# Performance work log

Hardware: AMD Instinct MI355X
Metric: run time of the kernel (lower is better)

The kernel has to match this reference:

```python
import jax, jax.numpy as jnp
import numpy as np

B_, S_, E_ = 1, 2048, 2048
NH, P_, N_, G_, K_, CS = 64, 64, 128, 1, 4, 256
INTER = NH * P_            # 4096
CONV_DIM = INTER + 2 * G_ * N_  # 4352
PROJ = INTER + CONV_DIM + NH
EPS = 1e-5


def setup_inputs() -> dict:
    key = jax.random.key(0)
    ks = jax.random.split(key, 6)
    return {
        "input_states": jax.random.normal(ks[0], (B_, S_, E_), dtype=jnp.float32),
        "mask": jnp.ones((B_, 1, S_), dtype=jnp.int32),
        "W_in": jax.random.normal(ks[1], (PROJ, E_), dtype=jnp.float32) * 0.02,
        "conv_w": jax.random.normal(ks[2], (CONV_DIM, K_), dtype=jnp.float32) * 0.2,
        "conv_b": jnp.zeros((CONV_DIM,), dtype=jnp.float32),
        "dt_bias": jnp.ones((NH,), dtype=jnp.float32),
        "A_log": jnp.log(jnp.arange(1, NH + 1, dtype=jnp.float32)),
        "D": jnp.ones((NH,), dtype=jnp.float32),
        "norm_w": jnp.ones((INTER,), dtype=jnp.float32),
        "W_out": jax.random.normal(ks[3], (E_, INTER), dtype=jnp.float32) * 0.02,
    }


def segsum(x):
    # x: [..., L]; out[..., i, j] = sum_{j < k <= i} x[..., k], -inf above diagonal
    L = x.shape[-1]
    i = jnp.arange(L)
    strict = i[:, None] > i[None, :]
    X = jnp.where(strict, x[..., :, None], 0.0)   # [..., L(i), L(j)]
    S = jnp.cumsum(X, axis=-2)
    return jnp.where(i[:, None] >= i[None, :], S, -jnp.inf)


def reference(input_states, mask, W_in, conv_w, conv_b, dt_bias, A_log, D, norm_w, W_out):
    B, S, E = input_states.shape
    # mask has shape[1]==1 -> apply_mask_to_padding_states is a no-op
    proj = input_states @ W_in.T                      # [B,S,PROJ]
    gate = proj[..., :INTER]
    h_BC = proj[..., INTER:INTER + CONV_DIM]
    dt = proj[..., INTER + CONV_DIM:]                 # [B,S,NH]

    # causal depthwise conv1d (padding=K-1, truncated to seq_len)
    xpad = jnp.pad(h_BC, ((0, 0), (K_ - 1, 0), (0, 0)))
    conv = conv_b
    for i in range(K_):
        conv = conv + xpad[:, i:i + S, :] * conv_w[:, i]
    h_BC = jax.nn.silu(conv)

    hidden = h_BC[..., :INTER]
    Bm = h_BC[..., INTER:INTER + G_ * N_]
    Cm = h_BC[..., INTER + G_ * N_:]

    A = -jnp.exp(A_log)                               # [NH]
    dt = jnp.clip(jax.nn.softplus(dt + dt_bias), 0.0) # [B,S,NH]

    Hs = hidden.reshape(B, S, NH, P_).astype(jnp.float32)
    Bm = jnp.tile(Bm.reshape(B, S, G_, N_).astype(jnp.float32), (1, 1, NH // G_, 1))
    Cm = jnp.tile(Cm.reshape(B, S, G_, N_).astype(jnp.float32), (1, 1, NH // G_, 1))

    D_resid = D[None, None, :, None] * Hs             # pad=0 since S % CS == 0
    Hdt = Hs * dt[..., None]
    At = A * dt                                       # [B,S,NH]

    C_ = S // CS
    Hc = Hdt.reshape(B, C_, CS, NH, P_)
    Ac = At.reshape(B, C_, CS, NH)
    Bc = Bm.reshape(B, C_, CS, NH, N_)
    Cc = Cm.reshape(B, C_, CS, NH, N_)

    Ap = jnp.transpose(Ac, (0, 3, 1, 2))              # [B,H,C,L]
    A_cum = jnp.cumsum(Ap, axis=-1)                   # [B,H,C,L]
    L_tri = jnp.exp(segsum(Ap))                       # [B,H,C,L,L]

    # diagonal (intra-chunk) output
    Gm = jnp.einsum('bclhn,bcshn->bclsh', Cc, Bc)
    M = Gm * jnp.transpose(L_tri, (0, 2, 3, 4, 1))    # [B,C,L,S,H]
    Yd = jnp.einsum('bclsh,bcshp->bclhp', M, Hc)

    # per-chunk states (note: source uses same-chunk states, no inter-chunk scan)
    decay = jnp.exp(A_cum[..., -1:] - A_cum)          # [B,H,C,L]
    Bd = Bc * jnp.transpose(decay, (0, 2, 3, 1))[..., None]
    states = jnp.einsum('bclhn,bclhp->bchpn', Bd, Hc) # [B,C,H,P,N]

    Sd = jnp.transpose(jnp.exp(A_cum), (0, 2, 3, 1))  # [B,C,L,H]
    Yoff = jnp.einsum('bclhn,bchpn->bclhp', Cc, states) * Sd[..., None]

    y = (Yd + Yoff).reshape(B, S, NH, P_) + D_resid
    y = y.reshape(B, S, INTER)

    # gated RMSNorm (fp32)
    yf = y.astype(jnp.float32) * jax.nn.silu(gate.astype(jnp.float32))
    var = jnp.mean(yf * yf, axis=-1, keepdims=True)
    yn = norm_w * (yf * jax.lax.rsqrt(var + EPS))

    return yn @ W_out.T
```

## Files before the change

### kernel.cpp

```cpp
#include <hip/hip_runtime.h>
#include <math.h>

#define S_LEN   2048
#define E_DIM   2048
#define NH      64
#define P_DIM   64
#define N_DIM   128
#define CS      256
#define NCHUNK  8
#define INTER   4096
#define CONVD   4352
#define PROJ    8512
#define GEMM1N  8448
#define EPS     1e-5f

#define OFF_PROJBF 0ull
#define OFF_HBC    8650752ull
#define OFF_DTG    13107200ull
#define OFF_DTPART 13238272ull
#define OFF_GM     17432576ull
#define OFF_YV     17956864ull
#define OFF_R      26345472ull
#define OFF_WOUT   37093376ull

typedef __bf16 bf16x8 __attribute__((ext_vector_type(8)));
typedef float  f32x4  __attribute__((ext_vector_type(4)));
typedef float  f32x16 __attribute__((ext_vector_type(16)));

__device__ __forceinline__ float bf2f(unsigned short u) {
    union { unsigned int i; float f; } v; v.i = ((unsigned int)u) << 16; return v.f;
}
__device__ __forceinline__ unsigned short f2bf(float f) {
    union { float f; unsigned int i; } v; v.f = f;
    unsigned int r = v.i + 0x7FFFu + ((v.i >> 16) & 1u);
    return (unsigned short)(r >> 16);
}
__device__ __forceinline__ void gl_lds16(const void* g, void* l) {
    __builtin_amdgcn_global_load_lds(
        (const __attribute__((address_space(1))) void*)g,
        (__attribute__((address_space(3))) void*)l, 16, 0, 0);
}

__global__ __launch_bounds__(256) void cast3_kernel(
    const float* __restrict__ X, const float* __restrict__ Win,
    const float* __restrict__ Wout, unsigned short* __restrict__ Xbf,
    unsigned short* __restrict__ Winbf, unsigned short* __restrict__ Woutbf)
{
    const int blk = blockIdx.x;
    const float* src; unsigned short* dst; size_t off;
    if (blk < 2048)       { src = X;    dst = Xbf;    off = (size_t)blk * 2048; }
    else if (blk < 10496) { src = Win;  dst = Winbf;  off = (size_t)(blk - 2048) * 2048; }
    else                  { src = Wout; dst = Woutbf; off = (size_t)(blk - 10496) * 2048; }
    size_t i = off + (size_t)threadIdx.x * 8;
    float4 a = *(const float4*)(src + i);
    float4 b = *(const float4*)(src + i + 4);
    uint4 o;
    o.x = (unsigned int)f2bf(a.x) | ((unsigned int)f2bf(a.y) << 16);
    o.y = (unsigned int)f2bf(a.z) | ((unsigned int)f2bf(a.w) << 16);
    o.z = (unsigned int)f2bf(b.x) | ((unsigned int)f2bf(b.y) << 16);
    o.w = (unsigned int)f2bf(b.z) | ((unsigned int)f2bf(b.w) << 16);
    *(uint4*)(dst + i) = o;
}

__global__ __launch_bounds__(256) void gemm_bt_mfma(
    const unsigned short* __restrict__ A, int lda, long long sA,
    const unsigned short* __restrict__ B, int ldb, long long sB,
    float* __restrict__ Cf, unsigned short* __restrict__ Cb, int ldc,
    long long sC, int K, int mswap)
{
    __shared__ unsigned short As[128 * 64];
    __shared__ unsigned short Bs[128 * 64];
    A += (long long)blockIdx.z * sA;
    B += (long long)blockIdx.z * sB;
    const int t     = threadIdx.x;
    const int m0    = (mswap ? blockIdx.x : blockIdx.y) * 128;
    const int n0    = (mswap ? blockIdx.y : blockIdx.x) * 128;
    const int w     = t >> 6;
    const int lane  = t & 63;
    const int col   = lane & 31;
    const int khalf = lane >> 5;
    const int wm    = (w & 1) * 64;
    const int wn    = (w >> 1) * 64;

    const int srow  = t >> 3;
    const int sslot = t & 7;
    const unsigned short* Agp[4];
    const unsigned short* Bgp[4];
#pragma unroll
    for (int i = 0; i < 4; i++) {
        const int r   = srow + 32 * i;
        const int gch = sslot ^ ((r ^ (r >> 3)) & 7);
        Agp[i] = A + (size_t)(m0 + r) * lda + gch * 8;
        Bgp[i] = B + (size_t)(n0 + r) * ldb + gch * 8;
    }
    unsigned short* Asl = &As[t * 8];
    unsigned short* Bsl = &Bs[t * 8];

    int aOff[2], aXor[2], bOff[2], bXor[2];
#pragma unroll
    for (int i = 0; i < 2; i++) {
        const int ra = wm + i * 32 + col;
        aOff[i] = ra * 64; aXor[i] = (ra ^ (ra >> 3)) & 7;
        const int rb = wn + i * 32 + col;
        bOff[i] = rb * 64; bXor[i] = (rb ^ (rb >> 3)) & 7;
    }

    f32x16 acc[2][2];
#pragma unroll
    for (int mi = 0; mi < 2; mi++)
#pragma unroll
        for (int ni = 0; ni < 2; ni++)
#pragma unroll
            for (int e = 0; e < 16; e++) acc[mi][ni][e] = 0.f;

    for (int k0 = 0; k0 < K; k0 += 64) {
        __syncthreads();
#pragma unroll
        for (int i = 0; i < 4; i++) {
            gl_lds16(Agp[i] + k0, Asl + i * 2048);
            gl_lds16(Bgp[i] + k0, Bsl + i * 2048);
        }
        __syncthreads();
#pragma unroll
        for (int ks = 0; ks < 4; ks++) {
            const int ch = ks * 2 + khalf;
            bf16x8 af[2], bfr[2];
#pragma unroll
            for (int i = 0; i < 2; i++) {
                af[i]  = *(const bf16x8*)&As[aOff[i] + ((ch ^ aXor[i]) * 8)];
                bfr[i] = *(const bf16x8*)&Bs[bOff[i] + ((ch ^ bXor[i]) * 8)];
            }
#pragma unroll
            for (int mi = 0; mi < 2; mi++)
#pragma unroll
                for (int ni = 0; ni < 2; ni++)
                    acc[mi][ni] = __builtin_amdgcn_mfma_f32_32x32x16_bf16(
                        af[mi], bfr[ni], acc[mi][ni], 0, 0, 0);
        }
    }

    if (Cb) {
#pragma unroll
        for (int mi = 0; mi < 2; mi++)
#pragma unroll
            for (int ni = 0; ni < 2; ni++) {
                const int rbase = m0 + wm + mi * 32 + 4 * khalf;
                const int cc    = n0 + wn + ni * 32 + col;
#pragma unroll
                for (int g = 0; g < 4; g++)
#pragma unroll
                    for (int rr = 0; rr < 4; rr++)
                        Cb[(size_t)(rbase + 8 * g + rr) * ldc + cc] =
                            f2bf(acc[mi][ni][4 * g + rr]);
            }
    } else {
        float* Cz = Cf + (long long)blockIdx.z * sC;
#pragma unroll
        for (int mi = 0; mi < 2; mi++)
#pragma unroll
            for (int ni = 0; ni < 2; ni++) {
                const int rbase = m0 + wm + mi * 32 + 4 * khalf;
                const int cc    = n0 + wn + ni * 32 + col;
#pragma unroll
                for (int g = 0; g < 4; g++)
#pragma unroll
                    for (int rr = 0; rr < 4; rr++)
                        Cz[(size_t)(rbase + 8 * g + rr) * ldc + cc] =
                            acc[mi][ni][4 * g + rr];
            }
    }
}

__global__ __launch_bounds__(256) void addf4_kernel(
    const float* __restrict__ p, float* __restrict__ o)
{
    size_t i = ((size_t)blockIdx.x * 256 + threadIdx.x) * 4;
    float4 a = *(const float4*)(p + i);
    float4 b = *(const float4*)(p + i + 4194304);
    float4 c = *(const float4*)(p + i + 8388608);
    float4 d = *(const float4*)(p + i + 12582912);
    float4 r = make_float4(a.x + b.x + c.x + d.x, a.y + b.y + c.y + d.y,
                           a.z + b.z + c.z + d.z, a.w + b.w + c.w + d.w);
    *(float4*)(o + i) = r;
}

__global__ __launch_bounds__(256) void gemm_nt(
    const float* __restrict__ A, int lda, long long sA,
    const float* __restrict__ B, int ldb, long long sB,
    float* __restrict__ C, int ldc, long long sC, int K)
{
    A += (long long)blockIdx.z * sA;
    B += (long long)blockIdx.z * sB;
    C += (long long)blockIdx.z * sC;
    const int t  = threadIdx.x;
    const int m0 = blockIdx.y * 128;
    const int n0 = blockIdx.x * 64;
    __shared__ float As[16][132];
    __shared__ float Bs[16][68];
    const int tx = t & 15;
    const int ty = t >> 4;

    const int arow = t & 127;
    const int akh  = (t >> 7) * 8;
    const float* Aload = A + (size_t)(m0 + arow) * (size_t)lda + akh;
    const int brow = t & 63;
    const int bk4  = (t >> 6) * 4;
    const float* Bload = B + (size_t)(n0 + brow) * (size_t)ldb + bk4;

    float acc[8][4];
#pragma unroll
    for (int i = 0; i < 8; i++)
#pragma unroll
        for (int j = 0; j < 4; j++) acc[i][j] = 0.f;

    for (int k0 = 0; k0 < K; k0 += 16) {
        __syncthreads();
        float4 a0 = *(const float4*)(Aload + k0);
        float4 a1 = *(const float4*)(Aload + k0 + 4);
        float4 b0 = *(const float4*)(Bload + k0);
        As[akh + 0][arow] = a0.x; As[akh + 1][arow] = a0.y;
        As[akh + 2][arow] = a0.z; As[akh + 3][arow] = a0.w;
        As[akh + 4][arow] = a1.x; As[akh + 5][arow] = a1.y;
        As[akh + 6][arow] = a1.z; As[akh + 7][arow] = a1.w;
        Bs[bk4 + 0][brow] = b0.x; Bs[bk4 + 1][brow] = b0.y;
        Bs[bk4 + 2][brow] = b0.z; Bs[bk4 + 3][brow] = b0.w;
        __syncthreads();
#pragma unroll
        for (int k = 0; k < 16; k++) {
            float4 a4 = *(const float4*)(&As[k][ty * 8]);
            float4 a5 = *(const float4*)(&As[k][ty * 8 + 4]);
            float4 b4 = *(const float4*)(&Bs[k][tx * 4]);
            float am[8] = {a4.x, a4.y, a4.z, a4.w, a5.x, a5.y, a5.z, a5.w};
            float bn[4] = {b4.x, b4.y, b4.z, b4.w};
#pragma unroll
            for (int i = 0; i < 8; i++)
#pragma unroll
                for (int j = 0; j < 4; j++) acc[i][j] += am[i] * bn[j];
        }
    }
#pragma unroll
    for (int i = 0; i < 8; i++) {
        float4 o = make_float4(acc[i][0], acc[i][1], acc[i][2], acc[i][3]);
        *(float4*)(C + (size_t)(m0 + ty * 8 + i) * (size_t)ldc + n0 + tx * 4) = o;
    }
}

__global__ __launch_bounds__(256) void dt_reduce_kernel(
    const float* __restrict__ part, const float* __restrict__ dt_bias,
    float* __restrict__ dtg)
{
    const int i = blockIdx.x * 256 + threadIdx.x;
    float x = dt_bias[i & 63];
#pragma unroll
    for (int z = 0; z < 32; z++) x += part[(size_t)z * 131072 + i];
    dtg[i] = (x > 20.f) ? x : log1pf(__expf(x));
}

__global__ __launch_bounds__(256) void conv_silu8_kernel(
    const unsigned short* __restrict__ projbf, const float* __restrict__ conv_w,
    const float* __restrict__ conv_b, unsigned short* __restrict__ out)
{
    const int c  = blockIdx.x * 256 + threadIdx.x;
    const int s0 = blockIdx.y * 8;
    const float4 w = *(const float4*)(conv_w + (size_t)c * 4);
    const float b = conv_b[c];
    const size_t base = 4096 + (size_t)c;
    float v[11];
#pragma unroll
    for (int m = 0; m < 11; m++) {
        int s = s0 - 3 + m;
        v[m] = (s >= 0) ? bf2f(projbf[(size_t)s * GEMM1N + base]) : 0.f;
    }
#pragma unroll
    for (int j = 0; j < 8; j++) {
        float acc = b + v[j] * w.x + v[j + 1] * w.y + v[j + 2] * w.z + v[j + 3] * w.w;
        float sig = 1.f / (1.f + __expf(-acc));
        out[(size_t)(s0 + j) * CONVD + c] = f2bf(acc * sig);
    }
}

__global__ __launch_bounds__(256, 2) void ssm_mfma_kernel(
    const unsigned short* __restrict__ hBC, const float* __restrict__ dtg,
    const float* __restrict__ Gm, const float* __restrict__ A_log,
    const float* __restrict__ Dp, float* __restrict__ y)
{
    const int h    = blockIdx.x;
    const int c    = blockIdx.y;
    const int t    = threadIdx.x;
    const int wid  = t >> 6;
    const int lane = t & 63;
    const int lo   = lane & 15;
    const int q    = lane >> 4;

    __shared__ float sAcum[CS], sdt[CS], sD[CS], sEs[CS], sDecay[CS], sScl[CS];
    __shared__ float sWaveSum[4];
    __shared__ unsigned short sHdtT[64 * 264];
    __shared__ unsigned short sStT[64 * 136];
    __shared__ unsigned short sBufB[128 * 72];

    const float A = -__expf(A_log[h]);
    const int row0 = c * CS;
    const unsigned short* hid = hBC + (size_t)row0 * CONVD + h * P_DIM;
    const unsigned short* Bp  = hBC + (size_t)row0 * CONVD + INTER;
    const unsigned short* Cp  = hBC + (size_t)row0 * CONVD + INTER + N_DIM;
    const float* gm = Gm + (size_t)c * CS * CS;

    float dtv = dtg[(size_t)(row0 + t) * NH + h];
    float v = A * dtv;
    for (int off = 1; off < 64; off <<= 1) {
        float u = __shfl_up(v, off, 64);
        if (lane >= off) v += u;
    }
    if (lane == 63) sWaveSum[wid] = v;
    __syncthreads();
    float pre = 0.f;
    for (int i = 0; i < 4; i++) if (i < wid) pre += sWaveSum[i];
    v += pre;
    sAcum[t] = v;
    sdt[t] = dtv;
    __syncthreads();
    const float AcumEnd = sAcum[CS - 1];
    {
        float ac   = sAcum[t];
        float apre = (t < 64) ? 0.f : sAcum[(t & ~63) - 1];
        sD[t]     = __expf(ac - apre);
        sEs[t]    = __expf(sAcum[t | 63] - ac);
        sDecay[t] = __expf(AcumEnd - ac);
        sScl[t]   = __expf(ac);
    }

    unsigned short* stgu = sStT;
    for (int lt = 0; lt < 4; lt++) {
        __syncthreads();
        {
            const int c8 = (t & 7) * 8;
#pragma unroll
            for (int j = 0; j < 2; j++) {
                int l = (t >> 3) + 32 * j;
                *(uint4*)&stgu[l * 64 + c8] =
                    *(const uint4*)(hid + (size_t)(lt * 64 + l) * CONVD + c8);
            }
        }
        __syncthreads();
        {
            const int p = t & 63, lq = (t >> 6) * 16;
#pragma unroll
            for (int j = 0; j < 4; j++) {
                ushort4 pk;
                int l0 = lq + j * 4;
                pk.x = f2bf(bf2f(stgu[(l0 + 0) * 64 + p]) * sdt[lt * 64 + l0 + 0]);
                pk.y = f2bf(bf2f(stgu[(l0 + 1) * 64 + p]) * sdt[lt * 64 + l0 + 1]);
                pk.z = f2bf(bf2f(stgu[(l0 + 2) * 64 + p]) * sdt[lt * 64 + l0 + 2]);
                pk.w = f2bf(bf2f(stgu[(l0 + 3) * 64 + p]) * sdt[lt * 64 + l0 + 3]);
                *(uint2*)&sHdtT[p * 264 + lt * 64 + l0] = *(uint2*)&pk;
            }
        }
    }

    f32x4 acc2[2][4];
#pragma unroll
    for (int mi = 0; mi < 2; mi++)
#pragma unroll
        for (int ni = 0; ni < 4; ni++) acc2[mi][ni] = (f32x4){0.f, 0.f, 0.f, 0.f};
    const int psub = (wid & 1) * 32;
    const int nsub = (wid >> 1) * 64;

    for (int qt = 0; qt < 4; qt++) {
        for (int hf = 0; hf < 2; hf++) {
            __syncthreads();
            {
                const int n8 = (t & 15) * 8;
#pragma unroll
                for (int j = 0; j < 2; j++) {
                    int r = (t >> 4) + 16 * j;
                    *(uint4*)&stgu[r * 128 + n8] =
                        *(const uint4*)(Bp + (size_t)(qt * 64 + hf * 32 + r) * CONVD + n8);
                }
            }
            __syncthreads();
            {
                const int n = t & 127, lc = (t >> 7) * 16;
#pragma unroll
                for (int j = 0; j < 4; j++) {
                    int l0 = lc + j * 4;
                    ushort4 pk;
                    pk.x = f2bf(bf2f(stgu[(l0 + 0) * 128 + n]) * sDecay[qt * 64 + hf * 32 + l0 + 0]);
                    pk.y = f2bf(bf2f(stgu[(l0 + 1) * 128 + n]) * sDecay[qt * 64 + hf * 32 + l0 + 1]);
                    pk.z = f2bf(bf2f(stgu[(l0 + 2) * 128 + n]) * sDecay[qt * 64 + hf * 32 + l0 + 2]);
                    pk.w = f2bf(bf2f(stgu[(l0 + 3) * 128 + n]) * sDecay[qt * 64 + hf * 32 + l0 + 3]);
                    *(uint2*)&sBufB[n * 72 + hf * 32 + l0] = *(uint2*)&pk;
                }
            }
        }
        __syncthreads();
#pragma unroll
        for (int ks = 0; ks < 2; ks++) {
            const int k0 = qt * 64 + ks * 32;
            const int kq = ks * 32;
            bf16x8 a2[2], b2[4];
#pragma unroll
            for (int mi = 0; mi < 2; mi++)
                a2[mi] = *(const bf16x8*)&sHdtT[(psub + mi * 16 + lo) * 264 + k0 + q * 8];
#pragma unroll
            for (int ni = 0; ni < 4; ni++)
                b2[ni] = *(const bf16x8*)&sBufB[(nsub + ni * 16 + lo) * 72 + kq + q * 8];
#pragma unroll
            for (int mi = 0; mi < 2; mi++)
#pragma unroll
                for (int ni = 0; ni < 4; ni++)
                    acc2[mi][ni] = __builtin_amdgcn_mfma_f32_16x16x32_bf16(
                        a2[mi], b2[ni], acc2[mi][ni], 0, 0, 0);
        }
    }
    __syncthreads();
#pragma unroll
    for (int mi = 0; mi < 2; mi++)
#pragma unroll
        for (int ni = 0; ni < 4; ni++)
#pragma unroll
            for (int rr = 0; rr < 4; rr++) {
                int p = psub + mi * 16 + q * 4 + rr;
                int n = nsub + ni * 16 + lo;
                sStT[p * 136 + n] = f2bf(acc2[mi][ni][rr]);
            }

    f32x4 accY[4][2][2];
#pragma unroll
    for (int i = 0; i < 4; i++)
#pragma unroll
        for (int mi = 0; mi < 2; mi++)
#pragma unroll
            for (int pi = 0; pi < 2; pi++) accY[i][mi][pi] = (f32x4){0.f, 0.f, 0.f, 0.f};
    const int pcol = (wid & 1) * 32;
    const int rsub = (wid >> 1) * 16;
    unsigned short* Cs = sBufB;

    for (int i = 0; i < 4; i++) {
        __syncthreads();
        {
            const int n8 = (t & 15) * 8;
#pragma unroll
            for (int j = 0; j < 4; j++) {
                int r = (t >> 4) + 16 * j;
                uint4 cv = *(const uint4*)(Cp + (size_t)(i * 64 + r) * CONVD + n8);
                float scl = sScl[i * 64 + r];
                const unsigned short* cu = (const unsigned short*)&cv;
                ushort4 p0, p1;
                p0.x = f2bf(bf2f(cu[0]) * scl); p0.y = f2bf(bf2f(cu[1]) * scl);
                p0.z = f2bf(bf2f(cu[2]) * scl); p0.w = f2bf(bf2f(cu[3]) * scl);
                p1.x = f2bf(bf2f(cu[4]) * scl); p1.y = f2bf(bf2f(cu[5]) * scl);
                p1.z = f2bf(bf2f(cu[6]) * scl); p1.w = f2bf(bf2f(cu[7]) * scl);
                *(uint2*)&Cs[r * 136 + n8]     = *(uint2*)&p0;
                *(uint2*)&Cs[r * 136 + n8 + 4] = *(uint2*)&p1;
            }
        }
        __syncthreads();
#pragma unroll
        for (int ks = 0; ks < 4; ks++) {
            const int k0 = ks * 32;
            bf16x8 a3[2], b3[2];
#pragma unroll
            for (int mi = 0; mi < 2; mi++)
                a3[mi] = *(const bf16x8*)&Cs[(mi * 32 + rsub + lo) * 136 + k0 + q * 8];
#pragma unroll
            for (int pi = 0; pi < 2; pi++)
                b3[pi] = *(const bf16x8*)&sStT[(pcol + pi * 16 + lo) * 136 + k0 + q * 8];
#pragma unroll
            for (int mi = 0; mi < 2; mi++)
#pragma unroll
                for (int pi = 0; pi < 2; pi++)
                    accY[i][mi][pi] = __builtin_amdgcn_mfma_f32_16x16x32_bf16(
                        a3[mi], b3[pi], accY[i][mi][pi], 0, 0, 0);
        }
    }

    unsigned short* Mt = sBufB;
    for (int i = 0; i < 4; i++) {
        const int nk = 2 * (i + 1);
        for (int mi = 0; mi < 2; mi++) {
            __syncthreads();
            if (wid <= i) {
                float P = 1.f;
                for (int m = wid + 1; m <= i - 1; m++) P *= sD[m * 64 + 63];
                const int s4 = wid * 64 + lo * 4;
                float4 es4 = *(const float4*)&sEs[s4];
#pragma unroll
                for (int j = 0; j < 8; j++) {
                    int lr = q + j * 4;
                    int l  = i * 64 + mi * 32 + lr;
                    float4 g4 = *(const float4*)&gm[(size_t)l * CS + s4];
                    float w0, w1, w2, w3;
                    if (wid == i) {
                        float al = sAcum[l];
                        w0 = (s4 + 0 <= l) ? __expf(al - sAcum[s4 + 0]) : 0.f;
                        w1 = (s4 + 1 <= l) ? __expf(al - sAcum[s4 + 1]) : 0.f;
                        w2 = (s4 + 2 <= l) ? __expf(al - sAcum[s4 + 2]) : 0.f;
                        w3 = (s4 + 3 <= l) ? __expf(al - sAcum[s4 + 3]) : 0.f;
                    } else {
                        float rs = sD[l] * P;
                        w0 = rs * es4.x; w1 = rs * es4.y;
                        w2 = rs * es4.z; w3 = rs * es4.w;
                    }
                    ushort4 pk;
                    pk.x = f2bf(g4.x * w0); pk.y = f2bf(g4.y * w1);
                    pk.z = f2bf(g4.z * w2); pk.w = f2bf(g4.w * w3);
                    *(uint2*)&Mt[lr * 264 + s4] = *(uint2*)&pk;
                }
            }
            __syncthreads();
            for (int ks = 0; ks < nk; ks++) {
                const int k0 = ks * 32;
                bf16x8 am = *(const bf16x8*)&Mt[(rsub + lo) * 264 + k0 + q * 8];
                bf16x8 b1[2];
#pragma unroll
                for (int pi = 0; pi < 2; pi++)
                    b1[pi] = *(const bf16x8*)&sHdtT[(pcol + pi * 16 + lo) * 264 + k0 + q * 8];
#pragma unroll
                for (int pi = 0; pi < 2; pi++)
                    accY[i][mi][pi] = __builtin_amdgcn_mfma_f32_16x16x32_bf16(
                        am, b1[pi], accY[i][mi][pi], 0, 0, 0);
            }
        }
    }

    const float Dh = Dp[h];
#pragma unroll
    for (int i = 0; i < 4; i++)
#pragma unroll
        for (int mi = 0; mi < 2; mi++)
#pragma unroll
            for (int pi = 0; pi < 2; pi++)
#pragma unroll
                for (int rr = 0; rr < 4; rr++) {
                    int l = i * 64 + mi * 32 + rsub + q * 4 + rr;
                    int p = pcol + pi * 16 + lo;
                    float hv = bf2f(hid[(size_t)l * CONVD + p]);
                    y[(size_t)(row0 + l) * INTER + h * P_DIM + p] =
                        accY[i][mi][pi][rr] + Dh * hv;
                }
}

__global__ __launch_bounds__(256) void norm_kernel(
    const float* __restrict__ y, const unsigned short* __restrict__ projbf,
    const float* __restrict__ norm_w, unsigned short* __restrict__ yn)
{
    const int s = blockIdx.x;
    const int t = threadIdx.x;
    __shared__ float sYf[INTER];
    __shared__ float sW[4];
    const float* yrow = y + (size_t)s * INTER;
    const unsigned short* grow = projbf + (size_t)s * GEMM1N;
    float sum = 0.f;
    for (int j0 = 0; j0 < INTER; j0 += 2048) {
        int j = j0 + t * 8;
        float4 y0 = *(const float4*)(yrow + j);
        float4 y1 = *(const float4*)(yrow + j + 4);
        uint4 gp = *(const uint4*)(grow + j);
        float gv[8] = {
            bf2f((unsigned short)(gp.x & 0xffff)), bf2f((unsigned short)(gp.x >> 16)),
            bf2f((unsigned short)(gp.y & 0xffff)), bf2f((unsigned short)(gp.y >> 16)),
            bf2f((unsigned short)(gp.z & 0xffff)), bf2f((unsigned short)(gp.z >> 16)),
            bf2f((unsigned short)(gp.w & 0xffff)), bf2f((unsigned short)(gp.w >> 16))};
        float yv8[8] = {y0.x, y0.y, y0.z, y0.w, y1.x, y1.y, y1.z, y1.w};
#pragma unroll
        for (int e = 0; e < 8; e++) {
            float f = yv8[e] * (gv[e] / (1.f + __expf(-gv[e])));
            sum += f * f;
            sYf[j + e] = f;
        }
    }
    for (int off = 32; off > 0; off >>= 1) sum += __shfl_down(sum, off, 64);
    if ((t & 63) == 0) sW[t >> 6] = sum;
    __syncthreads();
    const float var = (sW[0] + sW[1] + sW[2] + sW[3]) * (1.f / (float)INTER);
    const float rs = rsqrtf(var + EPS);
    for (int j0 = 0; j0 < INTER; j0 += 2048) {
        int j = j0 + t * 8;
        float4 w0 = *(const float4*)(norm_w + j);
        float4 w1 = *(const float4*)(norm_w + j + 4);
        float wv[8] = {w0.x, w0.y, w0.z, w0.w, w1.x, w1.y, w1.z, w1.w};
        unsigned short o[8];
#pragma unroll
        for (int e = 0; e < 8; e++) o[e] = f2bf(sYf[j + e] * wv[e] * rs);
        uint4 ov;
        ov.x = (unsigned int)o[0] | ((unsigned int)o[1] << 16);
        ov.y = (unsigned int)o[2] | ((unsigned int)o[3] << 16);
        ov.z = (unsigned int)o[4] | ((unsigned int)o[5] << 16);
        ov.w = (unsigned int)o[6] | ((unsigned int)o[7] << 16);
        *(uint4*)(yn + (size_t)s * INTER + j) = ov;
    }
}

extern "C" void kernel_launch(void* const* d_in, const int* in_sizes, int n_in,
                              void* d_out, int out_size, void* d_ws, size_t ws_size,
                              hipStream_t stream)
{
    const float* X       = (const float*)d_in[0];
    const float* W_in    = (const float*)d_in[2];
    const float* conv_w  = (const float*)d_in[3];
    const float* conv_b  = (const float*)d_in[4];
    const float* dt_bias = (const float*)d_in[5];
    const float* A_log   = (const float*)d_in[6];
    const float* Dp      = (const float*)d_in[7];
    const float* norm_w  = (const float*)d_in[8];
    const float* W_out   = (const float*)d_in[9];
    float* out = (float*)d_out;
    float* ws  = (float*)d_ws;

    unsigned short* projbf = (unsigned short*)(ws + OFF_PROJBF);
    unsigned short* hbc16  = (unsigned short*)(ws + OFF_HBC);
    float* dtg     = ws + OFF_DTG;
    float* dtpart  = ws + OFF_DTPART;
    float* gm      = ws + OFF_GM;
    float* yv      = ws + OFF_YV;
    unsigned short* Xbf    = (unsigned short*)(ws + OFF_R);
    unsigned short* Winbf  = (unsigned short*)(ws + OFF_R + 2097152);
    unsigned short* ynbf   = (unsigned short*)(ws + OFF_R);
    unsigned short* Woutbf = (unsigned short*)(ws + OFF_WOUT);
    float* part = ws;

    cast3_kernel<<<14592, 256, 0, stream>>>(X, W_in, W_out, Xbf, Winbf, Woutbf);

    gemm_bt_mfma<<<dim3(S_LEN / 128, GEMM1N / 128, 1), 256, 0, stream>>>(
        Xbf, E_DIM, 0LL, Winbf, E_DIM, 0LL, nullptr, projbf, GEMM1N, 0LL,
        E_DIM, 1);

    gemm_nt<<<dim3(1, 16, 32), 256, 0, stream>>>(
        X, E_DIM, 64LL, W_in + (size_t)GEMM1N * E_DIM, E_DIM, 64LL,
        dtpart, NH, 131072LL, 64);
    dt_reduce_kernel<<<512, 256, 0, stream>>>(dtpart, dt_bias, dtg);

    conv_silu8_kernel<<<dim3(CONVD / 256, S_LEN / 8), 256, 0, stream>>>(
        projbf, conv_w, conv_b, hbc16);

    gemm_bt_mfma<<<dim3(CS / 128, CS / 128, NCHUNK), 256, 0, stream>>>(
        hbc16 + INTER + N_DIM, CONVD, (long long)CS * CONVD,
        hbc16 + INTER,         CONVD, (long long)CS * CONVD,
        gm, nullptr, CS, (long long)CS * CS, N_DIM, 0);

    ssm_mfma_kernel<<<dim3(NH, NCHUNK), 256, 0, stream>>>(
        hbc16, dtg, gm, A_log, Dp, yv);

    norm_kernel<<<dim3(S_LEN), 256, 0, stream>>>(yv, projbf, norm_w, ynbf);

    gemm_bt_mfma<<<dim3(E_DIM / 128, S_LEN / 128, 4), 256, 0, stream>>>(
        ynbf, INTER, 1024LL, Woutbf, INTER, 1024LL,
        part, nullptr, E_DIM, 4194304LL, 1024, 0);
    addf4_kernel<<<4096, 256, 0, stream>>>(part, out);
}
```

Measured before the change: 424.9 us.

## Add 256x256-tile 8-wave GEMM with phased LDS pipelining for projections

Introduces a new bf16 MFMA GEMM kernel that uses 256x256 output tiles with 512 threads. It double-buffers 128KB of LDS with swizzled direct global-to-LDS loads and interleaves staging with four MMA phases per K-step, raising wave priority during MFMA bursts. The kernel replaces the 128x128 GEMM for both the input projection and the output projection, aiming for more data reuse per byte loaded and better overlap of memory with compute. The larger tiles leave fewer blocks (8x33 for GEMM1, 8x8x4 for the out projection), which may underfill the CUs. The 128KB shared allocation also limits occupancy.

```diff
diff --git a/kernel.cpp b/kernel.cpp
--- a/kernel.cpp
+++ b/kernel.cpp
@@ -60,6 +60,166 @@
     o.z = (unsigned int)f2bf(b.x) | ((unsigned int)f2bf(b.y) << 16);
     o.w = (unsigned int)f2bf(b.z) | ((unsigned int)f2bf(b.w) << 16);
     *(uint4*)(dst + i) = o;
+}
+
+#define WAITV(n) asm volatile("s_waitcnt vmcnt(" #n ")" ::: "memory")
+#define BARR()   asm volatile("s_barrier" ::: "memory")
+
+__global__ __launch_bounds__(512, 2) void gemm256_8ph(
+    const unsigned short* __restrict__ A, int lda, long long sA,
+    const unsigned short* __restrict__ B, int ldb, long long sB,
+    float* __restrict__ Cf, unsigned short* __restrict__ Cb, int ldc,
+    long long sC, int K, int mswap)
+{
+    __shared__ unsigned short sm[65536];
+    A += (long long)blockIdx.z * sA;
+    B += (long long)blockIdx.z * sB;
+    const int t    = threadIdx.x;
+    const int m0   = (mswap ? blockIdx.x : blockIdx.y) * 256;
+    const int n0   = (mswap ? blockIdx.y : blockIdx.x) * 256;
+    const int lane = t & 63;
+    const int w    = t >> 6;
+    const int wm   = ((w >> 2) & 1) * 64;
+    const int wn   = (w & 3) * 32;
+    const int l15  = lane & 15;
+    const int l4   = lane >> 4;
+    const int NT   = K >> 6;
+
+    const int sr = t >> 3, sl = t & 7;
+
+    auto STAGE = [&](int T, int h, int isB) {
+        const unsigned short* G = isB ? B : A;
+        const int ld   = isB ? ldb : lda;
+        const int base = (isB ? n0 : m0) + h * 128;
+        unsigned short* dst =
+            &sm[(T & 1) * 32768 + isB * 16384 + h * 8192 + t * 8];
+#pragma unroll
+        for (int j = 0; j < 2; j++) {
+            const int r   = sr + 64 * j;
+            const int gch = sl ^ ((r ^ (r >> 3)) & 7);
+            gl_lds16(G + (size_t)(base + r) * ld + T * 64 + gch * 8,
+                     dst + j * 4096);
+        }
+    };
+
+    int aoff[4], asw[4], boff[2], bsw[2];
+#pragma unroll
+    for (int mi = 0; mi < 4; mi++) {
+        int r = wm + mi * 16 + l15;
+        aoff[mi] = r * 64; asw[mi] = (r ^ (r >> 3)) & 7;
+    }
+#pragma unroll
+    for (int ni = 0; ni < 2; ni++) {
+        int r = wn + ni * 16 + l15;
+        boff[ni] = r * 64; bsw[ni] = (r ^ (r >> 3)) & 7;
+    }
+
+    bf16x8 aF[4][2], bF[2][2][2];
+    f32x4  acc[2][2][4][2];
+#pragma unroll
+    for (int qm = 0; qm < 2; qm++)
+#pragma unroll
+        for (int qn = 0; qn < 2; qn++)
+#pragma unroll
+            for (int mi = 0; mi < 4; mi++)
+#pragma unroll
+                for (int ni = 0; ni < 2; ni++)
+                    acc[qm][qn][mi][ni] = (f32x4){0.f, 0.f, 0.f, 0.f};
+
+#define LOAD_A(qm) do { \
+    const unsigned short* p_ = &sm[cb + (qm) * 8192]; \
+    _Pragma("unroll") for (int mi = 0; mi < 4; mi++) \
+    _Pragma("unroll") for (int ks = 0; ks < 2; ks++) \
+        aF[mi][ks] = *(const bf16x8*)&p_[aoff[mi] + \
+            (((ks * 4 + l4) ^ asw[mi]) << 3)]; \
+} while (0)
+#define LOAD_B(qn) do { \
+    const unsigned short* p_ = &sm[cb + 16384 + (qn) * 8192]; \
+    _Pragma("unroll") for (int ni = 0; ni < 2; ni++) \
+    _Pragma("unroll") for (int ks = 0; ks < 2; ks++) \
+        bF[qn][ni][ks] = *(const bf16x8*)&p_[boff[ni] + \
+            (((ks * 4 + l4) ^ bsw[ni]) << 3)]; \
+} while (0)
+#define MMA(qm, qn) do { \
+    __builtin_amdgcn_s_setprio(1); \
+    _Pragma("unroll") for (int ks = 0; ks < 2; ks++) \
+    _Pragma("unroll") for (int mi = 0; mi < 4; mi++) \
+    _Pragma("unroll") for (int ni = 0; ni < 2; ni++) \
+        acc[qm][qn][mi][ni] = __builtin_amdgcn_mfma_f32_16x16x32_bf16( \
+            aF[mi][ks], bF[qn][ni][ks], acc[qm][qn][mi][ni], 0, 0, 0); \
+    __builtin_amdgcn_s_setprio(0); \
+} while (0)
+
+    STAGE(0, 0, 0);
+    STAGE(0, 1, 1);
+    STAGE(0, 0, 1);
+    STAGE(0, 1, 0);
+    STAGE(1, 0, 0);
+    STAGE(1, 1, 1);
+    WAITV(0);
+    BARR();
+
+    for (int tt = 0; tt < NT; tt++) {
+        const int cb = (tt & 1) * 32768;
+        if (tt + 1 < NT) { WAITV(6); } else { WAITV(2); }
+        LOAD_A(0); LOAD_B(0);
+        if (tt + 1 < NT) STAGE(tt + 1, 0, 1);
+        BARR();
+        MMA(0, 0);
+        BARR();
+        LOAD_B(1);
+        if (tt + 1 < NT) STAGE(tt + 1, 1, 0);
+        BARR();
+        MMA(0, 1);
+        BARR();
+        if (tt + 1 < NT) { WAITV(6); } else { WAITV(0); }
+        LOAD_A(1);
+        if (tt + 2 < NT) STAGE(tt + 2, 0, 0);
+        BARR();
+        MMA(1, 1);
+        BARR();
+        if (tt + 2 < NT) STAGE(tt + 2, 1, 1);
+        BARR();
+        MMA(1, 0);
+        BARR();
+    }
+
+#undef LOAD_A
+#undef LOAD_B
+#undef MMA
+
+    if (Cb) {
+#pragma unroll
+        for (int qm = 0; qm < 2; qm++)
+#pragma unroll
+        for (int qn = 0; qn < 2; qn++)
+#pragma unroll
+        for (int mi = 0; mi < 4; mi++)
+#pragma unroll
+        for (int ni = 0; ni < 2; ni++) {
+            const int rb = m0 + qm * 128 + wm + mi * 16 + l4 * 4;
+            const int cc = n0 + qn * 128 + wn + ni * 16 + l15;
+#pragma unroll
+            for (int rr = 0; rr < 4; rr++)
+                Cb[(size_t)(rb + rr) * ldc + cc] = f2bf(acc[qm][qn][mi][ni][rr]);
+        }
+    } else {
+        float* Cz = Cf + (long long)blockIdx.z * sC;
+#pragma unroll
+        for (int qm = 0; qm < 2; qm++)
+#pragma unroll
+        for (int qn = 0; qn < 2; qn++)
+#pragma unroll
+        for (int mi = 0; mi < 4; mi++)
+#pragma unroll
+        for (int ni = 0; ni < 2; ni++) {
+            const int rb = m0 + qm * 128 + wm + mi * 16 + l4 * 4;
+            const int cc = n0 + qn * 128 + wn + ni * 16 + l15;
+#pragma unroll
+            for (int rr = 0; rr < 4; rr++)
+                Cz[(size_t)(rb + rr) * ldc + cc] = acc[qm][qn][mi][ni][rr];
+        }
+    }
 }
 
 __global__ __launch_bounds__(256) void gemm_bt_mfma(
@@ -621,7 +781,7 @@
 
     cast3_kernel<<<14592, 256, 0, stream>>>(X, W_in, W_out, Xbf, Winbf, Woutbf);
 
-    gemm_bt_mfma<<<dim3(S_LEN / 128, GEMM1N / 128, 1), 256, 0, stream>>>(
+    gemm256_8ph<<<dim3(S_LEN / 256, GEMM1N / 256, 1), 512, 0, stream>>>(
         Xbf, E_DIM, 0LL, Winbf, E_DIM, 0LL, nullptr, projbf, GEMM1N, 0LL,
         E_DIM, 1);
 
@@ -643,7 +803,7 @@
 
     norm_kernel<<<dim3(S_LEN), 256, 0, stream>>>(yv, projbf, norm_w, ynbf);
 
-    gemm_bt_mfma<<<dim3(E_DIM / 128, S_LEN / 128, 4), 256, 0, stream>>>(
+    gemm256_8ph<<<dim3(E_DIM / 256, S_LEN / 256, 4), 512, 0, stream>>>(
         ynbf, INTER, 1024LL, Woutbf, INTER, 1024LL,
         part, nullptr, E_DIM, 4194304LL, 1024, 0);
     addf4_kernel<<<4096, 256, 0, stream>>>(part, out);
```

Measured after the change: 457.7 us. 7.7% more time.
